# Kernel tuning notes

Measured on AMD Instinct MI355X. Metric: run time of the kernel, lower is better.

The kernel has to match this reference:

```python
import jax, jax.numpy as jnp
import numpy as np

B, T, C, S = 16, 32768, 64, 4  # batch, time, channels, n_sections


def setup_inputs() -> dict:
    key = jax.random.key(0)
    x = jax.random.normal(key, (B, T, C), dtype=jnp.float32)
    # Build STABLE biquad sections (random coeffs would blow up over 32k steps).
    rng = np.random.default_rng(0)
    r = rng.uniform(0.5, 0.9, S)                      # pole radius < 1 -> stable
    th = rng.uniform(0.1, np.pi - 0.1, S)             # pole angle
    a1 = -2.0 * r * np.cos(th)
    a2 = r ** 2
    b = rng.normal(0.0, 0.5, (S, 3))
    sos = np.concatenate([b, np.stack([np.ones(S), a1, a2], axis=1)], axis=1)
    return {"x": x, "sos": jnp.asarray(sos, dtype=jnp.float32)}


def _biquad(sig, b, a):
    # sig: [N, T]; direct-form-I recurrence, exactly the math of lfilter_bg with n_order=3:
    b0, b1, b2 = b[0], b[1], b[2]
    a0, a1, a2 = a[0], a[1], a[2]

    def step(carry, xt):
        x1, x2, y1, y2 = carry
        y = (b0 * xt + b1 * x1 + b2 * x2 - a1 * y1 - a2 * y2) / a0
        return (xt, x1, y, y1), y

    z = jnp.zeros((sig.shape[0],), sig.dtype)
    _, ys = jax.lax.scan(step, (z, z, z, z), sig.T)  # scan over time -> ys [T, N]
    return ys.T


def reference(x, sos):
    # x: [B, T, C] -> transpose(1,2) -> [B, C, T]; lfilter_bg flattens leading dims.
    Bb, Tt, Cc = x.shape
    sig = jnp.transpose(x, (0, 2, 1)).reshape(Bb * Cc, Tt)
    for s in range(sos.shape[0]):  # small fixed cascade of sections
        sig = _biquad(sig, sos[s, :3], sos[s, 3:])
    return jnp.transpose(sig.reshape(Bb, Cc, Tt), (0, 2, 1))
```

## Files before the change

kernel.cpp:

```cpp
#include <hip/hip_runtime.h>


#define TLEN  32768
#define CCH   64
#define BATCH 16
#define NSEC  4
#define CHUNK 256
#define WARM  320

#define NCHUNKS (TLEN / CHUNK)
#define NWAVES  (BATCH * NCHUNKS)
#define BLOCK   256
#define NBLOCKS (NWAVES * 64 / BLOCK)

__global__ __launch_bounds__(BLOCK) void sos_kernel(const float* __restrict__ x,
                                                    const float* __restrict__ sos,
                                                    float* __restrict__ out) {
    const int lane = threadIdx.x & 63;
    const int wid  = blockIdx.x * (BLOCK >> 6) + (threadIdx.x >> 6);
    const int b    = wid / NCHUNKS;
    const int k    = wid - b * NCHUNKS;
    const int t0   = k * CHUNK;
    const int s0   = (t0 >= WARM) ? (t0 - WARM) : 0;
    const int warm = t0 - s0;

    float c_b0[NSEC], c_b1[NSEC], c_b2[NSEC], c_a1n[NSEC], c_a2n[NSEC];
    float xx1[NSEC], xx2[NSEC], yy1[NSEC], yy2[NSEC];
#pragma unroll
    for (int s = 0; s < NSEC; ++s) {
        const float inva = 1.0f / sos[s * 6 + 3];
        c_b0[s]  =  sos[s * 6 + 0] * inva;
        c_b1[s]  =  sos[s * 6 + 1] * inva;
        c_b2[s]  =  sos[s * 6 + 2] * inva;
        c_a1n[s] = -sos[s * 6 + 4] * inva;
        c_a2n[s] = -sos[s * 6 + 5] * inva;
        xx1[s] = xx2[s] = yy1[s] = yy2[s] = 0.0f;
    }

    const float* __restrict__ px = x   + ((size_t)b * TLEN + (size_t)s0) * CCH + lane;
    float*       __restrict__ py = out + ((size_t)b * TLEN + (size_t)t0) * CCH + lane;

#pragma unroll 8
    for (int t = 0; t < warm; ++t) {
        float acc = *px; px += CCH;
#pragma unroll
        for (int s = 0; s < NSEC; ++s) {
            float y = fmaf(c_b0[s], acc,
                      fmaf(c_b1[s], xx1[s],
                      fmaf(c_b2[s], xx2[s],
                      fmaf(c_a1n[s], yy1[s], c_a2n[s] * yy2[s]))));
            xx2[s] = xx1[s]; xx1[s] = acc;
            yy2[s] = yy1[s]; yy1[s] = y;
            acc = y;
        }
    }

#pragma unroll 8
    for (int t = 0; t < CHUNK; ++t) {
        float acc = *px; px += CCH;
#pragma unroll
        for (int s = 0; s < NSEC; ++s) {
            float y = fmaf(c_b0[s], acc,
                      fmaf(c_b1[s], xx1[s],
                      fmaf(c_b2[s], xx2[s],
                      fmaf(c_a1n[s], yy1[s], c_a2n[s] * yy2[s]))));
            xx2[s] = xx1[s]; xx1[s] = acc;
            yy2[s] = yy1[s]; yy1[s] = y;
            acc = y;
        }
        *py = acc; py += CCH;
    }
}

extern "C" void kernel_launch(void* const* d_in, const int* in_sizes, int n_in,
                              void* d_out, int out_size, void* d_ws, size_t ws_size,
                              hipStream_t stream) {
    const float* x   = (const float*)d_in[0];
    const float* sos = (const float*)d_in[1];
    float* out = (float*)d_out;
    sos_kernel<<<NBLOCKS, BLOCK, 0, stream>>>(x, sos, out);
}
```

Before: 279.7 us.

## Skew biquad cascade across time steps and prefetch inputs in register blocks

Replaces the serial per-step cascade of four sections with a skewed pipeline. Each section processes a different time step, offset by one step from the previous section, so the four section updates within an iteration are independent and can issue in parallel rather than forming one long dependent FMA chain. Inputs are software-prefetched eight steps ahead into registers. Chunk and warm-up lengths are halved to 128, which doubles the number of waves and cuts redundant warm-up work, at the risk of reduced accuracy from the shorter warm-up. Writes become conditional inside the unrolled loop.

```diff
diff --git a/kernel.cpp b/kernel.cpp
--- a/kernel.cpp
+++ b/kernel.cpp
@@ -5,70 +5,84 @@
 #define CCH   64
 #define BATCH 16
 #define NSEC  4
-#define CHUNK 256
-#define WARM  320
+#define CHUNK 128
+#define WARM  128
+#define SKEW  3
 
 #define NCHUNKS (TLEN / CHUNK)
 #define NWAVES  (BATCH * NCHUNKS)
 #define BLOCK   256
 #define NBLOCKS (NWAVES * 64 / BLOCK)
 
-__global__ __launch_bounds__(BLOCK) void sos_kernel(const float* __restrict__ x,
-                                                    const float* __restrict__ sos,
-                                                    float* __restrict__ out) {
+__global__ __launch_bounds__(BLOCK, 4) void sos_kernel(const float* __restrict__ x,
+                                                       const float* __restrict__ sos,
+                                                       float* __restrict__ out) {
     const int lane = threadIdx.x & 63;
     const int wid  = blockIdx.x * (BLOCK >> 6) + (threadIdx.x >> 6);
-    const int b    = wid / NCHUNKS;
-    const int k    = wid - b * NCHUNKS;
+    const int b    = wid >> 8;
+    const int k    = wid & (NCHUNKS - 1);
     const int t0   = k * CHUNK;
     const int s0   = (t0 >= WARM) ? (t0 - WARM) : 0;
     const int warm = t0 - s0;
 
-    float c_b0[NSEC], c_b1[NSEC], c_b2[NSEC], c_a1n[NSEC], c_a2n[NSEC];
-    float xx1[NSEC], xx2[NSEC], yy1[NSEC], yy2[NSEC];
+    float cb0[NSEC], cb1[NSEC], cb2[NSEC], ca1[NSEC], ca2[NSEC];
+    float x1[NSEC], x2[NSEC], y1v[NSEC], y2v[NSEC];
 #pragma unroll
     for (int s = 0; s < NSEC; ++s) {
         const float inva = 1.0f / sos[s * 6 + 3];
-        c_b0[s]  =  sos[s * 6 + 0] * inva;
-        c_b1[s]  =  sos[s * 6 + 1] * inva;
-        c_b2[s]  =  sos[s * 6 + 2] * inva;
-        c_a1n[s] = -sos[s * 6 + 4] * inva;
-        c_a2n[s] = -sos[s * 6 + 5] * inva;
-        xx1[s] = xx2[s] = yy1[s] = yy2[s] = 0.0f;
+        cb0[s] =  sos[s * 6 + 0] * inva;
+        cb1[s] =  sos[s * 6 + 1] * inva;
+        cb2[s] =  sos[s * 6 + 2] * inva;
+        ca1[s] = -sos[s * 6 + 4] * inva;
+        ca2[s] = -sos[s * 6 + 5] * inva;
+        x1[s] = x2[s] = y1v[s] = y2v[s] = 0.0f;
+    }
+    float lat1 = 0.0f, lat2 = 0.0f, lat3 = 0.0f;
+
+    const float* __restrict__ xb = x + (size_t)b * TLEN * CCH + lane;
+    float* __restrict__ py = out + ((size_t)b * TLEN + (size_t)t0) * CCH + lane;
+
+    const int total  = warm + CHUNK + SKEW;
+    const int padded = (total + 7) & ~7;
+    const int sfrom  = warm + SKEW;
+
+    float xbuf[8];
+#pragma unroll
+    for (int j = 0; j < 8; ++j) {
+        int idx = s0 + j; if (idx > TLEN - 1) idx = TLEN - 1;
+        xbuf[j] = xb[(size_t)idx * CCH];
     }
 
-    const float* __restrict__ px = x   + ((size_t)b * TLEN + (size_t)s0) * CCH + lane;
-    float*       __restrict__ py = out + ((size_t)b * TLEN + (size_t)t0) * CCH + lane;
-
-#pragma unroll 8
-    for (int t = 0; t < warm; ++t) {
-        float acc = *px; px += CCH;
+    for (int g = 0; g < padded; g += 8) {
+        float nbuf[8];
 #pragma unroll
-        for (int s = 0; s < NSEC; ++s) {
-            float y = fmaf(c_b0[s], acc,
-                      fmaf(c_b1[s], xx1[s],
-                      fmaf(c_b2[s], xx2[s],
-                      fmaf(c_a1n[s], yy1[s], c_a2n[s] * yy2[s]))));
-            xx2[s] = xx1[s]; xx1[s] = acc;
-            yy2[s] = yy1[s]; yy1[s] = y;
-            acc = y;
+        for (int j = 0; j < 8; ++j) {
+            int idx = s0 + g + 8 + j; if (idx > TLEN - 1) idx = TLEN - 1;
+            nbuf[j] = xb[(size_t)idx * CCH];
         }
-    }
-
-#pragma unroll 8
-    for (int t = 0; t < CHUNK; ++t) {
-        float acc = *px; px += CCH;
 #pragma unroll
-        for (int s = 0; s < NSEC; ++s) {
-            float y = fmaf(c_b0[s], acc,
-                      fmaf(c_b1[s], xx1[s],
-                      fmaf(c_b2[s], xx2[s],
-                      fmaf(c_a1n[s], yy1[s], c_a2n[s] * yy2[s]))));
-            xx2[s] = xx1[s]; xx1[s] = acc;
-            yy2[s] = yy1[s]; yy1[s] = y;
-            acc = y;
+        for (int j = 0; j < 8; ++j) {
+            const int i = g + j;
+            const float i0 = xbuf[j], i1 = lat1, i2 = lat2, i3 = lat3;
+            const float p0 = fmaf(cb0[0], i0, fmaf(cb1[0], x1[0], cb2[0] * x2[0]));
+            const float p1 = fmaf(cb0[1], i1, fmaf(cb1[1], x1[1], cb2[1] * x2[1]));
+            const float p2 = fmaf(cb0[2], i2, fmaf(cb1[2], x1[2], cb2[2] * x2[2]));
+            const float p3 = fmaf(cb0[3], i3, fmaf(cb1[3], x1[3], cb2[3] * x2[3]));
+            const float o0 = fmaf(ca1[0], y1v[0], fmaf(ca2[0], y2v[0], p0));
+            const float o1 = fmaf(ca1[1], y1v[1], fmaf(ca2[1], y2v[1], p1));
+            const float o2 = fmaf(ca1[2], y1v[2], fmaf(ca2[2], y2v[2], p2));
+            const float o3 = fmaf(ca1[3], y1v[3], fmaf(ca2[3], y2v[3], p3));
+            x2[0] = x1[0]; x1[0] = i0;  y2v[0] = y1v[0]; y1v[0] = o0;
+            x2[1] = x1[1]; x1[1] = i1;  y2v[1] = y1v[1]; y1v[1] = o1;
+            x2[2] = x1[2]; x1[2] = i2;  y2v[2] = y1v[2]; y1v[2] = o2;
+            x2[3] = x1[3]; x1[3] = i3;  y2v[3] = y1v[3]; y1v[3] = o3;
+            lat1 = o0; lat2 = o1; lat3 = o2;
+            if (i >= sfrom && i < total) {
+                py[(size_t)(i - sfrom) * CCH] = o3;
+            }
         }
-        *py = acc; py += CCH;
+#pragma unroll
+        for (int j = 0; j < 8; ++j) xbuf[j] = nbuf[j];
     }
 }
 
```

New measurement: 259.5 us. -7.2%, faster.
